# Optimization experiments

Hardware: AMD Instinct MI355X
Metric: run time of the kernel (lower is better)

The kernel has to match this reference:

```python
import jax, jax.numpy as jnp
import numpy as np

N, E, G = 50000, 800000, 64
IN, EDGE = 128, 16
HID, H = 32, 4
FHID, HF = 64, 4
OUT = 16
NEG_SLOPE = 0.2


def _segment_softmax(logits, seg, num):
    m = jax.ops.segment_max(logits, seg, num_segments=num)
    m = jnp.where(jnp.isfinite(m), m, 0.0)
    p = jnp.exp(logits - m[seg])
    s = jax.ops.segment_sum(p, seg, num_segments=num)
    return p / (s[seg] + 1e-16)


def gatv2(x, src, dst, eattr, Wl, bl, Wr, br, We, att, bias, concat):
    # PyG GATv2Conv with add_self_loops=True (edge_attr fill_value='mean')
    n = x.shape[0]
    heads, ch = att.shape
    ones = jnp.ones((src.shape[0],), x.dtype)
    cnt = jax.ops.segment_sum(ones, dst, num_segments=n)
    mean_attr = jax.ops.segment_sum(eattr, dst, num_segments=n) / jnp.maximum(cnt, 1.0)[:, None]
    loop = jnp.arange(n)
    s = jnp.concatenate([src, loop])
    d = jnp.concatenate([dst, loop])
    ea = jnp.concatenate([eattr, mean_attr], axis=0)
    xl = (x @ Wl + bl).reshape(n, heads, ch)   # lin_l (source)
    xr = (x @ Wr + br).reshape(n, heads, ch)   # lin_r (target)
    ee = (ea @ We).reshape(-1, heads, ch)      # lin_edge (no bias)
    z = jax.nn.leaky_relu(xl[s] + xr[d] + ee, NEG_SLOPE)  # [E+N, H, C]
    logits = jnp.einsum('ehc,hc->eh', z, att)
    alpha = _segment_softmax(logits, d, n)
    out = jax.ops.segment_sum(alpha[:, :, None] * xl[s], d, num_segments=n)  # [N, H, C]
    out = out.reshape(n, heads * ch) if concat else out.mean(axis=1)
    return out + bias


def _forward(x, edge_attr, src, dst, batch,
             Wl0, bl0, Wr0, br0, We0, att0, bo0,
             Wlh, blh, Wrh, brh, Weh, atth, boh,
             Wlf, blf, Wrf, brf, Wef, attf, bof,
             Wlin, blin):
    h1 = jax.nn.relu(gatv2(x, src, dst, edge_attr, Wl0, bl0, Wr0, br0, We0, att0, bo0, True))
    h2 = jax.nn.relu(gatv2(h1, src, dst, edge_attr, Wlh, blh, Wrh, brh, Weh, atth, boh, True))
    h3 = jax.nn.relu(gatv2(h2, src, dst, edge_attr, Wlf, blf, Wrf, brf, Wef, attf, bof, False))
    # global_mean_pool over graphs
    gsum = jax.ops.segment_sum(h3, batch, num_segments=G)
    gcnt = jax.ops.segment_sum(jnp.ones((h3.shape[0],), h3.dtype), batch, num_segments=G)
    g = gsum / jnp.maximum(gcnt, 1.0)[:, None]
    return g @ Wlin + blin  # final_dropout inactive in eval mode


def setup_inputs():
    key = jax.random.key(0)
    ks = jax.random.split(key, 20)
    def p(i, shape, fan_in):
        return jax.random.normal(ks[i], shape, jnp.float32) / np.sqrt(fan_in)
    z = lambda *s: jnp.zeros(s, jnp.float32)
    return {
        'x': jax.random.normal(ks[0], (N, IN), jnp.float32),
        'edge_index': jax.random.randint(ks[1], (2, E), 0, N),
        'batch': jnp.sort(jax.random.randint(ks[2], (N,), 0, G)),
        'edge_attr': jax.random.normal(ks[3], (E, EDGE), jnp.float32),
        'Wl0': p(4, (IN, H * HID), IN), 'bl0': z(H * HID),
        'Wr0': p(5, (IN, H * HID), IN), 'br0': z(H * HID),
        'We0': p(6, (EDGE, H * HID), EDGE), 'att0': p(7, (H, HID), HID), 'bo0': z(H * HID),
        'Wlh': p(8, (H * HID, H * HID), H * HID), 'blh': z(H * HID),
        'Wrh': p(9, (H * HID, H * HID), H * HID), 'brh': z(H * HID),
        'Weh': p(10, (EDGE, H * HID), EDGE), 'atth': p(11, (H, HID), HID), 'boh': z(H * HID),
        'Wlf': p(12, (H * HID, HF * FHID), H * HID), 'blf': z(HF * FHID),
        'Wrf': p(13, (H * HID, HF * FHID), H * HID), 'brf': z(HF * FHID),
        'Wef': p(14, (EDGE, HF * FHID), EDGE), 'attf': p(15, (HF, FHID), FHID), 'bof': z(FHID),
        'Wlin': p(16, (FHID, OUT), FHID), 'blin': z(OUT),
    }


def reference(x, edge_index, batch, edge_attr, Wl0, bl0, Wr0, br0, We0, att0, bo0, Wlh, blh, Wrh, brh, Weh, atth, boh, Wlf, blf, Wrf, brf, Wef, attf, bof, Wlin, blin):
    return _forward(x, edge_attr, edge_index[0], edge_index[1], batch,
                    Wl0, bl0, Wr0, br0, We0, att0, bo0,
                    Wlh, blh, Wrh, brh, Weh, atth, boh,
                    Wlf, blf, Wrf, brf, Wef, attf, bof,
                    Wlin, blin)
```

## Files before the change

kernel.cpp:

```cpp
#include <hip/hip_runtime.h>
#include <cstddef>

#define NSLOPE 0.2f

constexpr int NN = 50000;
constexpr int EE = 800000;
constexpr int GG = 64;
constexpr int SCAN_B = 1024;

typedef unsigned short ushort_t;
typedef unsigned int uint_t;
typedef __bf16 bhalf;
typedef bhalf bhalf8 __attribute__((ext_vector_type(8)));
typedef float floatx4 __attribute__((ext_vector_type(4)));
typedef _Float16 half_t;
typedef half_t half2_t __attribute__((ext_vector_type(2)));

__device__ __forceinline__ ushort_t f2b(float f) {
  unsigned int u = __float_as_uint(f);
  unsigned int r = (u + 0x7fffu + ((u >> 16) & 1u)) >> 16;
  return (ushort_t)r;
}
__device__ __forceinline__ float b2f(ushort_t b) {
  return __uint_as_float(((unsigned int)b) << 16);
}
__device__ __forceinline__ uint_t packh2(float a, float b) {
  half2_t h = {(half_t)a, (half_t)b};
  return __builtin_bit_cast(uint_t, h);
}
__device__ __forceinline__ float dot2acc(uint_t ea, half2_t w, float c) {
  half2_t a = __builtin_bit_cast(half2_t, ea);
#if __has_builtin(__builtin_amdgcn_fdot2)
  return __builtin_amdgcn_fdot2(a, w, c, false);
#else
  return c + (float)a.x * (float)w.x + (float)a.y * (float)w.y;
#endif
}

__global__ void hist_kernel(const int* __restrict__ dst, int* __restrict__ hist, int E) {
  int e = blockIdx.x * blockDim.x + threadIdx.x;
  if (e < E) atomicAdd(&hist[dst[e]], 1);
}

__global__ void scan_block_kernel(const int* __restrict__ in, int* __restrict__ out,
                                  int* __restrict__ bsum, int n) {
  __shared__ int tmp[SCAN_B];
  int gid = blockIdx.x * SCAN_B + threadIdx.x;
  int v = (gid < n) ? in[gid] : 0;
  tmp[threadIdx.x] = v;
  __syncthreads();
  for (int off = 1; off < SCAN_B; off <<= 1) {
    int t = (threadIdx.x >= off) ? tmp[threadIdx.x - off] : 0;
    __syncthreads();
    tmp[threadIdx.x] += t;
    __syncthreads();
  }
  if (gid < n) out[gid] = tmp[threadIdx.x];
  if (threadIdx.x == SCAN_B - 1) bsum[blockIdx.x] = tmp[threadIdx.x];
}

__global__ void scan_totals_kernel(const int* __restrict__ bsum, int* __restrict__ boff, int nb) {
  if (blockIdx.x == 0 && threadIdx.x == 0) {
    int run = 0;
    for (int i = 0; i < nb; ++i) { boff[i] = run; run += bsum[i]; }
  }
}

__global__ void add_offsets_kernel(int* __restrict__ rowptr, const int* __restrict__ boff, int n) {
  int gid = blockIdx.x * SCAN_B + threadIdx.x;
  if (gid == 0) rowptr[0] = 0;
  if (gid < n) rowptr[1 + gid] += boff[blockIdx.x];
}

__global__ void copy_cursor_kernel(const int* __restrict__ rowptr, int* __restrict__ cursor, int n) {
  int i = blockIdx.x * blockDim.x + threadIdx.x;
  if (i < n) cursor[i] = rowptr[i];
}

__global__ void scatter_perm_kernel(const int* __restrict__ dst, int* __restrict__ cursor,
                                    int* __restrict__ perm, int E) {
  int e = blockIdx.x * blockDim.x + threadIdx.x;
  if (e < E) {
    int pos = atomicAdd(&cursor[dst[e]], 1);
    perm[pos] = e;
  }
}

__global__ void permute_kernel(const int* __restrict__ perm, const int* __restrict__ src,
                               const float* __restrict__ eattr,
                               int* __restrict__ srcp, uint_t* __restrict__ eah, int E) {
  int j = blockIdx.x * blockDim.x + threadIdx.x;
  if (j >= E) return;
  int e = perm[j];
  srcp[j] = src[e];
  const float* a = eattr + (size_t)e * 16;
  uint_t o[8];
#pragma unroll
  for (int k2 = 0; k2 < 8; ++k2) o[k2] = packh2(a[2 * k2], a[2 * k2 + 1]);
  uint4* b = reinterpret_cast<uint4*>(eah + (size_t)j * 8);
  b[0] = make_uint4(o[0], o[1], o[2], o[3]);
  b[1] = make_uint4(o[4], o[5], o[6], o[7]);
}

__global__ void mean_attr_kernel(const int* __restrict__ rowptr, const uint_t* __restrict__ eah,
                                 const int* __restrict__ perm, const float* __restrict__ eattr,
                                 int usePerm, uint_t* __restrict__ meanattr_h, int N) {
  int idx = blockIdx.x * blockDim.x + threadIdx.x;
  if (idx >= N * 8) return;
  int i = idx >> 3, k2 = idx & 7;
  int beg = rowptr[i], end = rowptr[i + 1];
  float ax = 0.f, ay = 0.f;
  if (!usePerm) {
    for (int j = beg; j < end; ++j) {
      half2_t h = __builtin_bit_cast(half2_t, eah[(size_t)j * 8 + k2]);
      ax += (float)h.x; ay += (float)h.y;
    }
  } else {
    for (int j = beg; j < end; ++j) {
      const float* ap = eattr + (size_t)perm[j] * 16 + k2 * 2;
      ax += ap[0]; ay += ap[1];
    }
  }
  int c = end - beg; if (c < 1) c = 1;
  float inv = 1.f / (float)c;
  meanattr_h[idx] = packh2(ax * inv, ay * inv);
}

__global__ void f2b_kernel(const float* __restrict__ in, ushort_t* __restrict__ out, int n4) {
  int i = blockIdx.x * blockDim.x + threadIdx.x;
  if (i >= n4) return;
  float4 v = reinterpret_cast<const float4*>(in)[i];
  ushort4 o = make_ushort4(f2b(v.x), f2b(v.y), f2b(v.z), f2b(v.w));
  reinterpret_cast<ushort4*>(out)[i] = o;
}

__global__ void prep_w_kernel(const float* W0, ushort_t* T0, int n0,
                              const float* W1, ushort_t* T1, int n1,
                              const float* W2, ushort_t* T2, int n2,
                              const float* W3, ushort_t* T3, int n3,
                              const float* W4, ushort_t* T4, int n4,
                              const float* W5, ushort_t* T5, int n5) {
  const float* W; ushort_t* T; int Nc;
  switch (blockIdx.y) {
    case 0: W = W0; T = T0; Nc = n0; break;
    case 1: W = W1; T = T1; Nc = n1; break;
    case 2: W = W2; T = T2; Nc = n2; break;
    case 3: W = W3; T = T3; Nc = n3; break;
    case 4: W = W4; T = T4; Nc = n4; break;
    default: W = W5; T = T5; Nc = n5; break;
  }
  int idx = blockIdx.x * blockDim.x + threadIdx.x;
  if (idx >= Nc * 128) return;
  int n = idx >> 7, k = idx & 127;
  T[idx] = f2b(W[(size_t)k * Nc + n]);
}

__global__ __launch_bounds__(256) void gemm_bt_dual_bf16(
    const ushort_t* __restrict__ Xb,
    const ushort_t* __restrict__ Wt0, const float* __restrict__ b0, ushort_t* __restrict__ Y0,
    const ushort_t* __restrict__ Wt1, const float* __restrict__ b1, ushort_t* __restrict__ Y1,
    int M, int Nc) {
  constexpr int K = 128, BM = 128, BN = 128, LDT = 136;
  __shared__ ushort_t Als[BM * LDT];
  __shared__ ushort_t Bls[BN * LDT];
  int nb = Nc >> 7;
  int half = blockIdx.y / nb;
  int cb = blockIdx.y % nb;
  const ushort_t* Wt = half ? Wt1 : Wt0;
  const float* bias = half ? b1 : b0;
  ushort_t* Y = half ? Y1 : Y0;
  int r0 = blockIdx.x * BM;
  int col0 = cb * BN;
  int tid = threadIdx.x;
  {
    int rl = tid >> 5;
    int kq = (tid & 31) * 4;
#pragma unroll
    for (int s = 0; s < 16; ++s) {
      int row = rl + s * 8;
      int grow = r0 + row;
      ushort4 v = make_ushort4(0, 0, 0, 0);
      if (grow < M) v = *reinterpret_cast<const ushort4*>(Xb + (size_t)grow * K + kq);
      *reinterpret_cast<ushort4*>(&Als[row * LDT + kq]) = v;
      ushort4 wv = *reinterpret_cast<const ushort4*>(Wt + (size_t)(col0 + row) * K + kq);
      *reinterpret_cast<ushort4*>(&Bls[row * LDT + kq]) = wv;
    }
  }
  __syncthreads();
  int lane = tid & 63;
  int w = tid >> 6;
  int m0 = (w >> 1) * 64;
  int n0 = (w & 1) * 64;
  int rin = lane & 15, quad = lane >> 4;
  floatx4 acc[4][4];
#pragma unroll
  for (int i = 0; i < 4; ++i)
#pragma unroll
    for (int j = 0; j < 4; ++j) acc[i][j] = (floatx4){0.f, 0.f, 0.f, 0.f};
#pragma unroll
  for (int kt = 0; kt < 4; ++kt) {
    int ko = kt * 32 + quad * 8;
    bhalf8 af[4], bf[4];
#pragma unroll
    for (int i = 0; i < 4; ++i)
      af[i] = *reinterpret_cast<const bhalf8*>(&Als[(m0 + i * 16 + rin) * LDT + ko]);
#pragma unroll
    for (int i = 0; i < 4; ++i)
      bf[i] = *reinterpret_cast<const bhalf8*>(&Bls[(n0 + i * 16 + rin) * LDT + ko]);
#pragma unroll
    for (int mi = 0; mi < 4; ++mi)
#pragma unroll
      for (int ni = 0; ni < 4; ++ni)
        acc[mi][ni] = __builtin_amdgcn_mfma_f32_16x16x32_bf16(af[mi], bf[ni], acc[mi][ni], 0, 0, 0);
  }
#pragma unroll
  for (int ni = 0; ni < 4; ++ni) {
    int gcol = col0 + n0 + ni * 16 + rin;
    float bb = bias[gcol];
#pragma unroll
    for (int mi = 0; mi < 4; ++mi) {
      int growb = r0 + m0 + mi * 16 + quad * 4;
#pragma unroll
      for (int r = 0; r < 4; ++r) {
        int grow = growb + r;
        if (grow < M) Y[(size_t)grow * Nc + gcol] = f2b(acc[mi][ni][r] + bb);
      }
    }
  }
}

template <int VPL>
__device__ __forceinline__ void loadb(const ushort_t* p, float* v) {
  if constexpr (VPL == 2) {
    ushort2 t = *reinterpret_cast<const ushort2*>(p);
    v[0] = b2f(t.x); v[1] = b2f(t.y);
  } else {
    ushort4 t = *reinterpret_cast<const ushort4*>(p);
    v[0] = b2f(t.x); v[1] = b2f(t.y); v[2] = b2f(t.z); v[3] = b2f(t.w);
  }
}
template <int VPL>
__device__ __forceinline__ void storeb(ushort_t* p, const float* v) {
  if constexpr (VPL == 2) {
    *reinterpret_cast<ushort2*>(p) = make_ushort2(f2b(v[0]), f2b(v[1]));
  } else {
    *reinterpret_cast<ushort4*>(p) = make_ushort4(f2b(v[0]), f2b(v[1]), f2b(v[2]), f2b(v[3]));
  }
}

template <int VPL>
__device__ __forceinline__ float lrelu_dot(const float* xv, const float* rv,
                                           const half2_t (*wepk)[VPL], const float* areg,
                                           const uint_t* ea) {
  float part = 0.f;
#pragma unroll
  for (int j = 0; j < VPL; ++j) {
    float z = xv[j] + rv[j];
#pragma unroll
    for (int k2 = 0; k2 < 8; ++k2) z = dot2acc(ea[k2], wepk[k2][j], z);
    float zl = fmaxf(z, NSLOPE * z);
    part = fmaf(zl, areg[j], part);
  }
  part += __shfl_xor(part, 1);
  part += __shfl_xor(part, 2);
  part += __shfl_xor(part, 4);
  part += __shfl_xor(part, 8);
  return part;
}

template <int EB, int VPL, int C>
__device__ __forceinline__ void process_group(
    const int* __restrict__ srcp, const uint_t* __restrict__ eah, int j,
    const ushort_t* __restrict__ xl, int lane, const float* rv,
    const half2_t (*wepk)[VPL], const float* areg,
    float& m, float& s, float* acc) {
  int sn[EB];
#pragma unroll
  for (int u = 0; u < EB; ++u) sn[u] = srcp[j + u];
  float xv[EB][VPL];
#pragma unroll
  for (int u = 0; u < EB; ++u) loadb<VPL>(xl + (size_t)sn[u] * C + lane * VPL, xv[u]);
  float lg[EB];
#pragma unroll
  for (int u = 0; u < EB; ++u) {
    const uint_t* ap = eah + (size_t)(j + u) * 8;
    uint_t ea[8];
#pragma unroll
    for (int k2 = 0; k2 < 8; ++k2) ea[k2] = ap[k2];
    lg[u] = lrelu_dot<VPL>(xv[u], rv, wepk, areg, ea);
  }
  float newm = m;
#pragma unroll
  for (int u = 0; u < EB; ++u) newm = fmaxf(newm, lg[u]);
  float sc = __expf(m - newm);
  float p[EB], ps = 0.f;
#pragma unroll
  for (int u = 0; u < EB; ++u) { p[u] = __expf(lg[u] - newm); ps += p[u]; }
  s = fmaf(s, sc, ps);
#pragma unroll
  for (int jj = 0; jj < VPL; ++jj) {
    float t = p[0] * xv[0][jj];
#pragma unroll
    for (int u = 1; u < EB; ++u) t = fmaf(p[u], xv[u][jj], t);
    acc[jj] = fmaf(acc[jj], sc, t);
  }
  m = newm;
}

template <int VPL, int C>
__device__ __forceinline__ void process_edge(
    int sn, const uint_t* ea,
    const ushort_t* __restrict__ xl, int lane, const float* rv,
    const half2_t (*wepk)[VPL], const float* areg,
    float& m, float& s, float* acc) {
  float xv[VPL];
  loadb<VPL>(xl + (size_t)sn * C + lane * VPL, xv);
  float lg = lrelu_dot<VPL>(xv, rv, wepk, areg, ea);
  float newm = fmaxf(m, lg);
  float sc = __expf(m - newm);
  float p = __expf(lg - newm);
  s = fmaf(s, sc, p);
#pragma unroll
  for (int jj = 0; jj < VPL; ++jj) acc[jj] = fmaf(acc[jj], sc, p * xv[jj]);
  m = newm;
}

template <int C, bool FINAL>
__global__ __launch_bounds__(256) void gat_fused_kernel(
    const int* __restrict__ rowptr,
    const int* __restrict__ srcp, const uint_t* __restrict__ eah,
    const int* __restrict__ perm, const int* __restrict__ src,
    const float* __restrict__ eattr, const uint_t* __restrict__ meanattr_h,
    int usePerm,
    const ushort_t* __restrict__ xl, const ushort_t* __restrict__ xr,
    const float* __restrict__ We,
    const float* __restrict__ att,
    const float* __restrict__ bias, ushort_t* __restrict__ hout, int N) {
  constexpr int VPL = C / 64;
  const int lane = threadIdx.x & 63;
  int d = __builtin_amdgcn_readfirstlane(blockIdx.x * (blockDim.x >> 6) + (threadIdx.x >> 6));
  if (d >= N) return;

  half2_t wepk[8][VPL];
  float areg[VPL];
#pragma unroll
  for (int k2 = 0; k2 < 8; ++k2)
#pragma unroll
    for (int j = 0; j < VPL; ++j) {
      int ch = lane * VPL + j;
      wepk[k2][j] = (half2_t){(half_t)We[(2 * k2) * C + ch], (half_t)We[(2 * k2 + 1) * C + ch]};
    }
#pragma unroll
  for (int j = 0; j < VPL; ++j) areg[j] = att[lane * VPL + j];

  int beg = rowptr[d], end = rowptr[d + 1];
  float rv[VPL];
  loadb<VPL>(xr + (size_t)d * C + lane * VPL, rv);

  float m = -INFINITY, s = 0.f;
  float acc[VPL];
#pragma unroll
  for (int j = 0; j < VPL; ++j) acc[j] = 0.f;

  if (!usePerm) {
    int j = beg;
    if constexpr (C == 128) {
      for (; j + 8 <= end; j += 8)
        process_group<8, VPL, C>(srcp, eah, j, xl, lane, rv, wepk, areg, m, s, acc);
    }
    for (; j + 4 <= end; j += 4)
      process_group<4, VPL, C>(srcp, eah, j, xl, lane, rv, wepk, areg, m, s, acc);
    for (; j + 2 <= end; j += 2)
      process_group<2, VPL, C>(srcp, eah, j, xl, lane, rv, wepk, areg, m, s, acc);
    for (; j < end; ++j)
      process_group<1, VPL, C>(srcp, eah, j, xl, lane, rv, wepk, areg, m, s, acc);
  } else {
    for (int j = beg; j < end; ++j) {
      int e = perm[j];
      int sn = src[e];
      const float* ap = eattr + (size_t)e * 16;
      uint_t ea[8];
#pragma unroll
      for (int k2 = 0; k2 < 8; ++k2) ea[k2] = packh2(ap[2 * k2], ap[2 * k2 + 1]);
      process_edge<VPL, C>(sn, ea, xl, lane, rv, wepk, areg, m, s, acc);
    }
  }
  {
    const uint_t* mp = meanattr_h + (size_t)d * 8;
    uint_t ea[8];
#pragma unroll
    for (int k2 = 0; k2 < 8; ++k2) ea[k2] = mp[k2];
    process_edge<VPL, C>(d, ea, xl, lane, rv, wepk, areg, m, s, acc);
  }

  float inv = 1.f / (s + 1e-16f);
  if constexpr (!FINAL) {
    float res[VPL];
#pragma unroll
    for (int j = 0; j < VPL; ++j) {
      float v = acc[j] * inv + bias[lane * VPL + j];
      res[j] = v > 0.f ? v : 0.f;
    }
    storeb<VPL>(hout + (size_t)d * C + lane * VPL, res);
  } else {
    float v[VPL];
#pragma unroll
    for (int j = 0; j < VPL; ++j) v[j] = acc[j] * inv;
#pragma unroll
    for (int j = 0; j < VPL; ++j) {
      v[j] += __shfl_xor(v[j], 16);
      v[j] += __shfl_xor(v[j], 32);
    }
    if (lane < 16) {
      float res[VPL];
#pragma unroll
      for (int j = 0; j < VPL; ++j) {
        float val = 0.25f * v[j] + bias[lane * VPL + j];
        res[j] = val > 0.f ? val : 0.f;
      }
      storeb<VPL>(hout + (size_t)d * 64 + lane * VPL, res);
    }
  }
}

__global__ __launch_bounds__(256) void pool_kernel(
    const ushort_t* __restrict__ h3, const int* __restrict__ batch,
    float* __restrict__ gsum, float* __restrict__ gcnt, int N) {
  const int lane = threadIdx.x & 63;
  const int w = blockIdx.x * (blockDim.x >> 6) + (threadIdx.x >> 6);
  const int nw = gridDim.x * (blockDim.x >> 6);
  const int chunk = (N + nw - 1) / nw;
  int i0 = w * chunk;
  int i1 = i0 + chunk; if (i1 > N) i1 = N;
  if (i0 >= i1) return;
  int cur = batch[i0];
  float acc = 0.f;
  int cnt = 0;
  for (int i = i0; i < i1; ++i) {
    int g = batch[i];
    if (g != cur) {
      atomicAdd(&gsum[(size_t)cur * 64 + lane], acc);
      if (lane == 0) atomicAdd(&gcnt[cur], (float)cnt);
      acc = 0.f; cnt = 0; cur = g;
    }
    acc += b2f(h3[(size_t)i * 64 + lane]);
    ++cnt;
  }
  atomicAdd(&gsum[(size_t)cur * 64 + lane], acc);
  if (lane == 0) atomicAdd(&gcnt[cur], (float)cnt);
}

__global__ void final_kernel(const float* __restrict__ gsum, const float* __restrict__ gcnt,
                             const float* __restrict__ Wlin, const float* __restrict__ blin,
                             float* __restrict__ out) {
  int idx = blockIdx.x * blockDim.x + threadIdx.x;
  if (idx >= GG * 16) return;
  int g = idx >> 4, o = idx & 15;
  float c = gcnt[g];
  c = c > 1.f ? c : 1.f;
  float inv = 1.f / c;
  float acc = blin[o];
  for (int f = 0; f < 64; ++f) acc = fmaf(gsum[(size_t)g * 64 + f] * inv, Wlin[f * 16 + o], acc);
  out[idx] = acc;
}

extern "C" void kernel_launch(void* const* d_in, const int* in_sizes, int n_in,
                              void* d_out, int out_size, void* d_ws, size_t ws_size,
                              hipStream_t stream) {
  (void)in_sizes; (void)n_in; (void)out_size;
  const float* x     = (const float*)d_in[0];
  const int*   eidx  = (const int*)d_in[1];
  const int*   batch = (const int*)d_in[2];
  const float* eattr = (const float*)d_in[3];
  const float* Wl0 = (const float*)d_in[4];  const float* bl0 = (const float*)d_in[5];
  const float* Wr0 = (const float*)d_in[6];  const float* br0 = (const float*)d_in[7];
  const float* We0 = (const float*)d_in[8];  const float* att0 = (const float*)d_in[9];
  const float* bo0 = (const float*)d_in[10];
  const float* Wlh = (const float*)d_in[11]; const float* blh = (const float*)d_in[12];
  const float* Wrh = (const float*)d_in[13]; const float* brh = (const float*)d_in[14];
  const float* Weh = (const float*)d_in[15]; const float* atth = (const float*)d_in[16];
  const float* boh = (const float*)d_in[17];
  const float* Wlf = (const float*)d_in[18]; const float* blf = (const float*)d_in[19];
  const float* Wrf = (const float*)d_in[20]; const float* brf = (const float*)d_in[21];
  const float* Wef = (const float*)d_in[22]; const float* attf = (const float*)d_in[23];
  const float* bof = (const float*)d_in[24];
  const float* Wlin = (const float*)d_in[25]; const float* blin = (const float*)d_in[26];

  const int* src = eidx;
  const int* dst = eidx + EE;

  char* ws = (char*)d_ws;
  size_t off = 0;
  auto take = [&](size_t bytes) -> void* {
    void* p = ws + off;
    off += (bytes + 1023) & ~(size_t)1023;
    return p;
  };
  ushort_t* xl     = (ushort_t*)take((size_t)NN * 256 * 2);
  ushort_t* xr     = (ushort_t*)take((size_t)NN * 256 * 2);
  ushort_t* hb     = (ushort_t*)take((size_t)NN * 128 * 2);
  ushort_t* xb     = (ushort_t*)take((size_t)NN * 128 * 2);
  uint_t* meanattr_h = (uint_t*)take((size_t)NN * 8 * 4);
  int* hist        = (int*)take((size_t)NN * 4);
  int* rowptr      = (int*)take((size_t)(NN + 1) * 4);
  int* cursor      = (int*)take((size_t)NN * 4);
  int* perm        = (int*)take((size_t)EE * 4);
  int* bsum        = (int*)take(256);
  int* boff        = (int*)take(256);
  float* gsum      = (float*)take((size_t)GG * 64 * 4);
  float* gcnt      = (float*)take((size_t)GG * 4);
  ushort_t* wtl0   = (ushort_t*)take((size_t)128 * 128 * 2);
  ushort_t* wtr0   = (ushort_t*)take((size_t)128 * 128 * 2);
  ushort_t* wtlh   = (ushort_t*)take((size_t)128 * 128 * 2);
  ushort_t* wtrh   = (ushort_t*)take((size_t)128 * 128 * 2);
  ushort_t* wtlf   = (ushort_t*)take((size_t)256 * 128 * 2);
  ushort_t* wtrf   = (ushort_t*)take((size_t)256 * 128 * 2);
  size_t perm_need = off + (((size_t)EE * 4 + 1023) & ~(size_t)1023)
                   + (((size_t)EE * 8 * 4 + 1023) & ~(size_t)1023);
  int usePerm = (ws_size >= perm_need) ? 0 : 1;
  int* srcp = nullptr; uint_t* eah = nullptr;
  if (!usePerm) {
    srcp = (int*)take((size_t)EE * 4);
    eah  = (uint_t*)take((size_t)EE * 8 * 4);
  }

  hipMemsetAsync(hist, 0, (size_t)NN * 4, stream);
  hipMemsetAsync(gsum, 0, (size_t)GG * 64 * 4, stream);
  hipMemsetAsync(gcnt, 0, (size_t)GG * 4, stream);
  hist_kernel<<<(EE + 255) / 256, 256, 0, stream>>>(dst, hist, EE);
  int nsb = (NN + SCAN_B - 1) / SCAN_B;
  scan_block_kernel<<<nsb, SCAN_B, 0, stream>>>(hist, rowptr + 1, bsum, NN);
  scan_totals_kernel<<<1, 64, 0, stream>>>(bsum, boff, nsb);
  add_offsets_kernel<<<nsb, SCAN_B, 0, stream>>>(rowptr, boff, NN);
  copy_cursor_kernel<<<(NN + 255) / 256, 256, 0, stream>>>(rowptr, cursor, NN);
  scatter_perm_kernel<<<(EE + 255) / 256, 256, 0, stream>>>(dst, cursor, perm, EE);
  if (!usePerm)
    permute_kernel<<<(EE + 255) / 256, 256, 0, stream>>>(perm, src, eattr, srcp, eah, EE);
  mean_attr_kernel<<<(NN * 8 + 255) / 256, 256, 0, stream>>>(rowptr, eah, perm, eattr,
                                                             usePerm, meanattr_h, NN);
  prep_w_kernel<<<dim3(128, 6), 256, 0, stream>>>(Wl0, wtl0, 128, Wr0, wtr0, 128,
                                                  Wlh, wtlh, 128, Wrh, wtrh, 128,
                                                  Wlf, wtlf, 256, Wrf, wtrf, 256);
  f2b_kernel<<<(NN * 128 / 4 + 255) / 256, 256, 0, stream>>>(x, xb, NN * 128 / 4);

  const int AGG_BLOCKS = (NN + 3) / 4;
  const int GEMM_MB = (NN + 127) / 128;

  gemm_bt_dual_bf16<<<dim3(GEMM_MB, 2), 256, 0, stream>>>(xb, wtl0, bl0, xl, wtr0, br0, xr, NN, 128);
  gat_fused_kernel<128, false><<<AGG_BLOCKS, 256, 0, stream>>>(
      rowptr, srcp, eah, perm, src, eattr, meanattr_h, usePerm, xl, xr, We0, att0, bo0, hb, NN);
  gemm_bt_dual_bf16<<<dim3(GEMM_MB, 2), 256, 0, stream>>>(hb, wtlh, blh, xl, wtrh, brh, xr, NN, 128);
  gat_fused_kernel<128, false><<<AGG_BLOCKS, 256, 0, stream>>>(
      rowptr, srcp, eah, perm, src, eattr, meanattr_h, usePerm, xl, xr, Weh, atth, boh, hb, NN);
  gemm_bt_dual_bf16<<<dim3(GEMM_MB, 4), 256, 0, stream>>>(hb, wtlf, blf, xl, wtrf, brf, xr, NN, 256);
  gat_fused_kernel<256, true><<<AGG_BLOCKS, 256, 0, stream>>>(
      rowptr, srcp, eah, perm, src, eattr, meanattr_h, usePerm, xl, xr, Wef, attf, bof, hb, NN);
  pool_kernel<<<128, 256, 0, stream>>>(hb, batch, gsum, gcnt, NN);
  final_kernel<<<4, 256, 0, stream>>>(gsum, gcnt, Wlin, blin, (float*)d_out);
}
```

Before: 727.8 us.

## Drop online-softmax max tracking, fuse cursor copy into scan offsets, remove perm fallback

```diff
diff --git a/kernel.cpp b/kernel.cpp
--- a/kernel.cpp
+++ b/kernel.cpp
@@ -66,15 +66,15 @@
   }
 }
 
-__global__ void add_offsets_kernel(int* __restrict__ rowptr, const int* __restrict__ boff, int n) {
+__global__ void add_offsets_kernel(int* __restrict__ rowptr, const int* __restrict__ boff,
+                                   int* __restrict__ cursor, int n) {
   int gid = blockIdx.x * SCAN_B + threadIdx.x;
-  if (gid == 0) rowptr[0] = 0;
-  if (gid < n) rowptr[1 + gid] += boff[blockIdx.x];
-}
-
-__global__ void copy_cursor_kernel(const int* __restrict__ rowptr, int* __restrict__ cursor, int n) {
-  int i = blockIdx.x * blockDim.x + threadIdx.x;
-  if (i < n) cursor[i] = rowptr[i];
+  if (gid == 0) { rowptr[0] = 0; cursor[0] = 0; }
+  if (gid < n) {
+    int v = rowptr[1 + gid] + boff[blockIdx.x];
+    rowptr[1 + gid] = v;
+    if (1 + gid < n) cursor[1 + gid] = v;
+  }
 }
 
 __global__ void scatter_perm_kernel(const int* __restrict__ dst, int* __restrict__ cursor,
@@ -103,23 +103,15 @@
 }
 
 __global__ void mean_attr_kernel(const int* __restrict__ rowptr, const uint_t* __restrict__ eah,
-                                 const int* __restrict__ perm, const float* __restrict__ eattr,
-                                 int usePerm, uint_t* __restrict__ meanattr_h, int N) {
+                                 uint_t* __restrict__ meanattr_h, int N) {
   int idx = blockIdx.x * blockDim.x + threadIdx.x;
   if (idx >= N * 8) return;
   int i = idx >> 3, k2 = idx & 7;
   int beg = rowptr[i], end = rowptr[i + 1];
   float ax = 0.f, ay = 0.f;
-  if (!usePerm) {
-    for (int j = beg; j < end; ++j) {
-      half2_t h = __builtin_bit_cast(half2_t, eah[(size_t)j * 8 + k2]);
-      ax += (float)h.x; ay += (float)h.y;
-    }
-  } else {
-    for (int j = beg; j < end; ++j) {
-      const float* ap = eattr + (size_t)perm[j] * 16 + k2 * 2;
-      ax += ap[0]; ay += ap[1];
-    }
+  for (int j = beg; j < end; ++j) {
+    half2_t h = __builtin_bit_cast(half2_t, eah[(size_t)j * 8 + k2]);
+    ax += (float)h.x; ay += (float)h.y;
   }
   int c = end - beg; if (c < 1) c = 1;
   float inv = 1.f / (float)c;
@@ -160,9 +152,9 @@
     const ushort_t* __restrict__ Wt0, const float* __restrict__ b0, ushort_t* __restrict__ Y0,
     const ushort_t* __restrict__ Wt1, const float* __restrict__ b1, ushort_t* __restrict__ Y1,
     int M, int Nc) {
-  constexpr int K = 128, BM = 128, BN = 128, LDT = 136;
+  constexpr int K = 128, BM = 128, LDT = 136;
   __shared__ ushort_t Als[BM * LDT];
-  __shared__ ushort_t Bls[BN * LDT];
+  __shared__ ushort_t Bls[BM * LDT];
   int nb = Nc >> 7;
   int half = blockIdx.y / nb;
   int cb = blockIdx.y % nb;
@@ -170,7 +162,7 @@
   const float* bias = half ? b1 : b0;
   ushort_t* Y = half ? Y1 : Y0;
   int r0 = blockIdx.x * BM;
-  int col0 = cb * BN;
+  int col0 = cb * 128;
   int tid = threadIdx.x;
   {
     int rl = tid >> 5;
@@ -273,7 +265,7 @@
     const int* __restrict__ srcp, const uint_t* __restrict__ eah, int j,
     const ushort_t* __restrict__ xl, int lane, const float* rv,
     const half2_t (*wepk)[VPL], const float* areg,
-    float& m, float& s, float* acc) {
+    float& s, float* acc) {
   int sn[EB];
 #pragma unroll
   for (int u = 0; u < EB; ++u) sn[u] = srcp[j + u];
@@ -289,22 +281,17 @@
     for (int k2 = 0; k2 < 8; ++k2) ea[k2] = ap[k2];
     lg[u] = lrelu_dot<VPL>(xv[u], rv, wepk, areg, ea);
   }
-  float newm = m;
-#pragma unroll
-  for (int u = 0; u < EB; ++u) newm = fmaxf(newm, lg[u]);
-  float sc = __expf(m - newm);
   float p[EB], ps = 0.f;
 #pragma unroll
-  for (int u = 0; u < EB; ++u) { p[u] = __expf(lg[u] - newm); ps += p[u]; }
-  s = fmaf(s, sc, ps);
+  for (int u = 0; u < EB; ++u) { p[u] = __expf(lg[u]); ps += p[u]; }
+  s += ps;
 #pragma unroll
   for (int jj = 0; jj < VPL; ++jj) {
     float t = p[0] * xv[0][jj];
 #pragma unroll
     for (int u = 1; u < EB; ++u) t = fmaf(p[u], xv[u][jj], t);
-    acc[jj] = fmaf(acc[jj], sc, t);
-  }
-  m = newm;
+    acc[jj] += t;
+  }
 }
 
 template <int VPL, int C>
@@ -312,26 +299,21 @@
     int sn, const uint_t* ea,
     const ushort_t* __restrict__ xl, int lane, const float* rv,
     const half2_t (*wepk)[VPL], const float* areg,
-    float& m, float& s, float* acc) {
+    float& s, float* acc) {
   float xv[VPL];
   loadb<VPL>(xl + (size_t)sn * C + lane * VPL, xv);
   float lg = lrelu_dot<VPL>(xv, rv, wepk, areg, ea);
-  float newm = fmaxf(m, lg);
-  float sc = __expf(m - newm);
-  float p = __expf(lg - newm);
-  s = fmaf(s, sc, p);
-#pragma unroll
-  for (int jj = 0; jj < VPL; ++jj) acc[jj] = fmaf(acc[jj], sc, p * xv[jj]);
-  m = newm;
+  float p = __expf(lg);
+  s += p;
+#pragma unroll
+  for (int jj = 0; jj < VPL; ++jj) acc[jj] = fmaf(p, xv[jj], acc[jj]);
 }
 
 template <int C, bool FINAL>
 __global__ __launch_bounds__(256) void gat_fused_kernel(
     const int* __restrict__ rowptr,
     const int* __restrict__ srcp, const uint_t* __restrict__ eah,
-    const int* __restrict__ perm, const int* __restrict__ src,
-    const float* __restrict__ eattr, const uint_t* __restrict__ meanattr_h,
-    int usePerm,
+    const uint_t* __restrict__ meanattr_h,
     const ushort_t* __restrict__ xl, const ushort_t* __restrict__ xr,
     const float* __restrict__ We,
     const float* __restrict__ att,
@@ -357,66 +339,54 @@
   float rv[VPL];
   loadb<VPL>(xr + (size_t)d * C + lane * VPL, rv);
 
-  float m = -INFINITY, s = 0.f;
+  float s = 0.f;
   float acc[VPL];
 #pragma unroll
   for (int j = 0; j < VPL; ++j) acc[j] = 0.f;
 
-  if (!usePerm) {
-    int j = beg;
-    if constexpr (C == 128) {
-      for (; j + 8 <= end; j += 8)
-        process_group<8, VPL, C>(srcp, eah, j, xl, lane, rv, wepk, areg, m, s, acc);
-    }
-    for (; j + 4 <= end; j += 4)
-      process_group<4, VPL, C>(srcp, eah, j, xl, lane, rv, wepk, areg, m, s, acc);
-    for (; j + 2 <= end; j += 2)
-      process_group<2, VPL, C>(srcp, eah, j, xl, lane, rv, wepk, areg, m, s, acc);
-    for (; j < end; ++j)
-      process_group<1, VPL, C>(srcp, eah, j, xl, lane, rv, wepk, areg, m, s, acc);
-  } else {
-    for (int j = beg; j < end; ++j) {
-      int e = perm[j];
-      int sn = src[e];
-      const float* ap = eattr + (size_t)e * 16;
-      uint_t ea[8];
-#pragma unroll
-      for (int k2 = 0; k2 < 8; ++k2) ea[k2] = packh2(ap[2 * k2], ap[2 * k2 + 1]);
-      process_edge<VPL, C>(sn, ea, xl, lane, rv, wepk, areg, m, s, acc);
-    }
-  }
+  int j = beg;
+  if constexpr (C == 128) {
+    for (; j + 8 <= end; j += 8)
+      process_group<8, VPL, C>(srcp, eah, j, xl, lane, rv, wepk, areg, s, acc);
+  }
+  for (; j + 4 <= end; j += 4)
+    process_group<4, VPL, C>(srcp, eah, j, xl, lane, rv, wepk, areg, s, acc);
+  for (; j + 2 <= end; j += 2)
+    process_group<2, VPL, C>(srcp, eah, j, xl, lane, rv, wepk, areg, s, acc);
+  for (; j < end; ++j)
+    process_group<1, VPL, C>(srcp, eah, j, xl, lane, rv, wepk, areg, s, acc);
   {
     const uint_t* mp = meanattr_h + (size_t)d * 8;
     uint_t ea[8];
 #pragma unroll
     for (int k2 = 0; k2 < 8; ++k2) ea[k2] = mp[k2];
-    process_edge<VPL, C>(d, ea, xl, lane, rv, wepk, areg, m, s, acc);
+    process_edge<VPL, C>(d, ea, xl, lane, rv, wepk, areg, s, acc);
   }
 
   float inv = 1.f / (s + 1e-16f);
   if constexpr (!FINAL) {
     float res[VPL];
 #pragma unroll
-    for (int j = 0; j < VPL; ++j) {
-      float v = acc[j] * inv + bias[lane * VPL + j];
-      res[j] = v > 0.f ? v : 0.f;
+    for (int jj = 0; jj < VPL; ++jj) {
+      float v = acc[jj] * inv + bias[lane * VPL + jj];
+      res[jj] = v > 0.f ? v : 0.f;
     }
     storeb<VPL>(hout + (size_t)d * C + lane * VPL, res);
   } else {
     float v[VPL];
 #pragma unroll
-    for (int j = 0; j < VPL; ++j) v[j] = acc[j] * inv;
-#pragma unroll
-    for (int j = 0; j < VPL; ++j) {
-      v[j] += __shfl_xor(v[j], 16);
-      v[j] += __shfl_xor(v[j], 32);
+    for (int jj = 0; jj < VPL; ++jj) v[jj] = acc[jj] * inv;
+#pragma unroll
+    for (int jj = 0; jj < VPL; ++jj) {
+      v[jj] += __shfl_xor(v[jj], 16);
+      v[jj] += __shfl_xor(v[jj], 32);
     }
     if (lane < 16) {
       float res[VPL];
 #pragma unroll
-      for (int j = 0; j < VPL; ++j) {
-        float val = 0.25f * v[j] + bias[lane * VPL + j];
-        res[j] = val > 0.f ? val : 0.f;
+      for (int jj = 0; jj < VPL; ++jj) {
+        float val = 0.25f * v[jj] + bias[lane * VPL + jj];
+        res[jj] = val > 0.f ? val : 0.f;
       }
       storeb<VPL>(hout + (size_t)d * 64 + lane * VPL, res);
     }
@@ -467,7 +437,7 @@
 extern "C" void kernel_launch(void* const* d_in, const int* in_sizes, int n_in,
                               void* d_out, int out_size, void* d_ws, size_t ws_size,
                               hipStream_t stream) {
-  (void)in_sizes; (void)n_in; (void)out_size;
+  (void)in_sizes; (void)n_in; (void)out_size; (void)ws_size;
   const float* x     = (const float*)d_in[0];
   const int*   eidx  = (const int*)d_in[1];
   const int*   batch = (const int*)d_in[2];
@@ -515,14 +485,8 @@
   ushort_t* wtrh   = (ushort_t*)take((size_t)128 * 128 * 2);
   ushort_t* wtlf   = (ushort_t*)take((size_t)256 * 128 * 2);
   ushort_t* wtrf   = (ushort_t*)take((size_t)256 * 128 * 2);
-  size_t perm_need = off + (((size_t)EE * 4 + 1023) & ~(size_t)1023)
-                   + (((size_t)EE * 8 * 4 + 1023) & ~(size_t)1023);
-  int usePerm = (ws_size >= perm_need) ? 0 : 1;
-  int* srcp = nullptr; uint_t* eah = nullptr;
-  if (!usePerm) {
-    srcp = (int*)take((size_t)EE * 4);
-    eah  = (uint_t*)take((size_t)EE * 8 * 4);
-  }
+  int* srcp        = (int*)take((size_t)EE * 4);
+  uint_t* eah      = (uint_t*)take((size_t)EE * 8 * 4);
 
   hipMemsetAsync(hist, 0, (size_t)NN * 4, stream);
   hipMemsetAsync(gsum, 0, (size_t)GG * 64 * 4, stream);
@@ -531,13 +495,10 @@
   int nsb = (NN + SCAN_B - 1) / SCAN_B;
   scan_block_kernel<<<nsb, SCAN_B, 0, stream>>>(hist, rowptr + 1, bsum, NN);
   scan_totals_kernel<<<1, 64, 0, stream>>>(bsum, boff, nsb);
-  add_offsets_kernel<<<nsb, SCAN_B, 0, stream>>>(rowptr, boff, NN);
-  copy_cursor_kernel<<<(NN + 255) / 256, 256, 0, stream>>>(rowptr, cursor, NN);
+  add_offsets_kernel<<<nsb, SCAN_B, 0, stream>>>(rowptr, boff, cursor, NN);
   scatter_perm_kernel<<<(EE + 255) / 256, 256, 0, stream>>>(dst, cursor, perm, EE);
-  if (!usePerm)
-    permute_kernel<<<(EE + 255) / 256, 256, 0, stream>>>(perm, src, eattr, srcp, eah, EE);
-  mean_attr_kernel<<<(NN * 8 + 255) / 256, 256, 0, stream>>>(rowptr, eah, perm, eattr,
-                                                             usePerm, meanattr_h, NN);
+  permute_kernel<<<(EE + 255) / 256, 256, 0, stream>>>(perm, src, eattr, srcp, eah, EE);
+  mean_attr_kernel<<<(NN * 8 + 255) / 256, 256, 0, stream>>>(rowptr, eah, meanattr_h, NN);
   prep_w_kernel<<<dim3(128, 6), 256, 0, stream>>>(Wl0, wtl0, 128, Wr0, wtr0, 128,
                                                   Wlh, wtlh, 128, Wrh, wtrh, 128,
                                                   Wlf, wtlf, 256, Wrf, wtrf, 256);
@@ -548,13 +509,13 @@
 
   gemm_bt_dual_bf16<<<dim3(GEMM_MB, 2), 256, 0, stream>>>(xb, wtl0, bl0, xl, wtr0, br0, xr, NN, 128);
   gat_fused_kernel<128, false><<<AGG_BLOCKS, 256, 0, stream>>>(
-      rowptr, srcp, eah, perm, src, eattr, meanattr_h, usePerm, xl, xr, We0, att0, bo0, hb, NN);
+      rowptr, srcp, eah, meanattr_h, xl, xr, We0, att0, bo0, hb, NN);
   gemm_bt_dual_bf16<<<dim3(GEMM_MB, 2), 256, 0, stream>>>(hb, wtlh, blh, xl, wtrh, brh, xr, NN, 128);
   gat_fused_kernel<128, false><<<AGG_BLOCKS, 256, 0, stream>>>(
-      rowptr, srcp, eah, perm, src, eattr, meanattr_h, usePerm, xl, xr, Weh, atth, boh, hb, NN);
+      rowptr, srcp, eah, meanattr_h, xl, xr, Weh, atth, boh, hb, NN);
   gemm_bt_dual_bf16<<<dim3(GEMM_MB, 4), 256, 0, stream>>>(hb, wtlf, blf, xl, wtrf, brf, xr, NN, 256);
   gat_fused_kernel<256, true><<<AGG_BLOCKS, 256, 0, stream>>>(
-      rowptr, srcp, eah, perm, src, eattr, meanattr_h, usePerm, xl, xr, Wef, attf, bof, hb, NN);
+      rowptr, srcp, eah, meanattr_h, xl, xr, Wef, attf, bof, hb, NN);
   pool_kernel<<<128, 256, 0, stream>>>(hb, batch, gsum, gcnt, NN);
   final_kernel<<<4, 256, 0, stream>>>(gsum, gcnt, Wlin, blin, (float*)d_out);
 }
```

Result: no change. 717.9 us (-1.4%).
